# Performance work log

Hardware: AMD Instinct MI355X
Metric: run time of the kernel (lower is better)

The kernel has to match this reference:

```python
import jax, jax.numpy as jnp
import numpy as np

N_HEAD = 16
N_EMBD = 1024


def setup_inputs() -> dict:
    key = jax.random.key(0)
    k1, k2 = jax.random.split(key)
    x = jax.random.normal(k1, (2, 2048, N_EMBD), dtype=jnp.float32)
    # nn.Linear(n_embd, 3*n_embd, bias=False); store as [in, out] for x @ w
    w_qkv = jax.random.normal(k2, (N_EMBD, 3 * N_EMBD), dtype=jnp.float32) * (N_EMBD ** -0.5)
    return {"x": x, "w_qkv": w_qkv}


def reference(x, w_qkv):
    B, T, C = x.shape
    H = N_HEAD
    D = C // H  # head dim
    qkv = x @ w_qkv  # [B, T, 3C]
    q, k, v = jnp.split(qkv, 3, axis=2)
    # [B, T, H, D] -> [B, H, T, D]
    q = q.reshape(B, T, H, D).transpose(0, 2, 1, 3)
    k = k.reshape(B, T, H, D).transpose(0, 2, 1, 3)
    v = v.reshape(B, T, H, D).transpose(0, 2, 1, 3)
    att = jnp.einsum('bhtd,bhsd->bhts', q, k) / np.sqrt(D).astype(np.float32)
    causal = jnp.tril(jnp.ones((T, T), dtype=bool))  # [T, T]
    att = jnp.where(causal, att, -jnp.inf)
    att = jax.nn.softmax(att, axis=-1)
    out = jnp.einsum('bhts,bhsd->bhtd', att, v)  # [B, H, T, D]
    return out.transpose(0, 2, 1, 3).reshape(B, T, C)
```

## Files before the change

### kernel.cpp

```cpp
#include <hip/hip_runtime.h>
#include <hip/hip_bf16.h>

#define BATCH 2
#define SEQ   2048
#define EMBD  1024
#define NHEAD 16
#define HDIM  64
#define N3    3072
#define MTOT  4096
#define KDIM  1024

typedef __attribute__((ext_vector_type(8))) short  short8;
typedef __attribute__((ext_vector_type(4))) short  s16x4;
typedef __attribute__((ext_vector_type(4))) float  f32x4;

__device__ __forceinline__ short f2bfs(float f) {
    return __builtin_bit_cast(short, __float2bfloat16(f));
}

__global__ __launch_bounds__(256) void cast_x_kernel(const float* __restrict__ x,
                                                     short* __restrict__ xb, int n4) {
    int i = blockIdx.x * 256 + threadIdx.x;
    if (i >= n4) return;
    float4 f = reinterpret_cast<const float4*>(x)[i];
    s16x4 o;
    o[0] = f2bfs(f.x); o[1] = f2bfs(f.y);
    o[2] = f2bfs(f.z); o[3] = f2bfs(f.w);
    reinterpret_cast<s16x4*>(xb)[i] = o;
}

__global__ __launch_bounds__(256) void cast_wt_kernel(const float* __restrict__ w,
                                                      short* __restrict__ wt) {
    __shared__ float tile[32][33];
    int n0 = blockIdx.x * 32;
    int k0 = blockIdx.y * 32;
    int tx = threadIdx.x & 31;
    int ty = threadIdx.x >> 5;
#pragma unroll
    for (int i = 0; i < 4; ++i)
        tile[ty + i * 8][tx] = w[(size_t)(k0 + ty + i * 8) * N3 + n0 + tx];
    __syncthreads();
#pragma unroll
    for (int i = 0; i < 4; ++i)
        wt[(size_t)(n0 + ty + i * 8) * KDIM + k0 + tx] = f2bfs(tile[tx][ty + i * 8]);
}

__device__ __forceinline__ void stage_tile(const short* gbase, short* lbase, int tid) {
#pragma unroll
    for (int c = 0; c < 2; ++c) {
        int row = c * 64 + (tid >> 2);
        int chunk = (tid & 3) ^ ((row >> 1) & 3);
        const short* gp = gbase + (size_t)row * KDIM + chunk * 8;
        short* lp = lbase + c * 2048 + tid * 8;
        __builtin_amdgcn_global_load_lds((const __attribute__((address_space(1))) void*)gp,
                                         (__attribute__((address_space(3))) void*)lp,
                                         16, 0, 0);
    }
}

__global__ __launch_bounds__(256) void qkv_gemm_kernel(const short* __restrict__ xb,
                                                       const short* __restrict__ wt,
                                                       short* __restrict__ qb,
                                                       short* __restrict__ kbuf,
                                                       short* __restrict__ vt) {
    __shared__ short lA[2][128 * 32];
    __shared__ short lB[2][128 * 32];

    const int tid  = threadIdx.x;
    const int lane = tid & 63;
    const int wid  = tid >> 6;
    const int wm = wid >> 1, wn = wid & 1;
    const int lid = blockIdx.x;
    const int swz = (lid & 7) * 96 + (lid >> 3);
    const int m0 = (swz / 24) * 128;
    const int n0 = (swz % 24) * 128;

    f32x4 acc[4][4];
#pragma unroll
    for (int i = 0; i < 4; ++i)
#pragma unroll
        for (int j = 0; j < 4; ++j) acc[i][j] = (f32x4){0.f, 0.f, 0.f, 0.f};

    const short* gA = xb + (size_t)m0 * KDIM;
    const short* gB = wt + (size_t)n0 * KDIM;

    stage_tile(gA, lA[0], tid);
    stage_tile(gB, lB[0], tid);

    int cur = 0;
    const int arow = (lane & 15) * 32 + (((lane >> 4) ^ ((lane >> 1) & 3)) * 8);
#pragma unroll 1
    for (int kt = 0; kt < KDIM / 32; ++kt) {
        if (kt + 1 < KDIM / 32) {
            stage_tile(gA + (kt + 1) * 32, lA[cur ^ 1], tid);
            stage_tile(gB + (kt + 1) * 32, lB[cur ^ 1], tid);
            asm volatile("s_waitcnt vmcnt(4)" ::: "memory");
        } else {
            asm volatile("s_waitcnt vmcnt(0)" ::: "memory");
        }
        __builtin_amdgcn_s_barrier();
        __builtin_amdgcn_sched_barrier(0);
        short8 a[4], b[4];
#pragma unroll
        for (int im = 0; im < 4; ++im)
            a[im] = *(const short8*)&lA[cur][(wm * 64 + im * 16) * 32 + arow];
#pragma unroll
        for (int in = 0; in < 4; ++in)
            b[in] = *(const short8*)&lB[cur][(wn * 64 + in * 16) * 32 + arow];
#pragma unroll
        for (int im = 0; im < 4; ++im)
#pragma unroll
            for (int in = 0; in < 4; ++in)
                acc[im][in] = __builtin_amdgcn_mfma_f32_16x16x32_bf16(a[im], b[in], acc[im][in], 0, 0, 0);
        __builtin_amdgcn_sched_barrier(0);
        __builtin_amdgcn_s_barrier();
        cur ^= 1;
    }

#pragma unroll
    for (int im = 0; im < 4; ++im) {
        int t0m = m0 + wm * 64 + im * 16 + (lane >> 4) * 4;
        int b = t0m >> 11;
        int t0 = t0m & 2047;
#pragma unroll
        for (int in = 0; in < 4; ++in) {
            int col = n0 + wn * 64 + in * 16 + (lane & 15);
            int which = col >> 10;
            int h = (col >> 6) & 15;
            int d = col & 63;
            if (which == 2) {
                s16x4 pk;
#pragma unroll
                for (int r = 0; r < 4; ++r) pk[r] = f2bfs(acc[im][in][r]);
                *(s16x4*)&vt[((size_t)(b * NHEAD + h) * HDIM + d) * SEQ + t0] = pk;
            } else {
                short* dst = (which == 0) ? qb : kbuf;
                float sc = (which == 0) ? 0.125f : 1.0f;
#pragma unroll
                for (int r = 0; r < 4; ++r)
                    dst[((size_t)(b * NHEAD + h) * SEQ + t0 + r) * HDIM + d] = f2bfs(acc[im][in][r] * sc);
            }
        }
    }
}

#define KVB 128

__device__ __forceinline__ int swzf(int r) { return (r & 3) ^ (((r >> 2) & 3) << 1); }

__device__ __forceinline__ void stage_kv(const short* kh, const short* vh, int kb,
                                         short* lk, short* lv, int tid) {
#pragma unroll
    for (int c = 0; c < 2; ++c) {
        int row = c * 64 + (tid >> 3);
        int sch = (tid & 7) ^ swzf(row);
        const short* gk = kh + (size_t)(kb + row) * HDIM + sch * 8;
        __builtin_amdgcn_global_load_lds((const __attribute__((address_space(1))) void*)gk,
                                         (__attribute__((address_space(3))) void*)(lk + c * 4096 + tid * 8), 16, 0, 0);
    }
#pragma unroll
    for (int c = 0; c < 2; ++c) {
        int d = c * 32 + (tid >> 4);
        int sch = (tid & 15) ^ (d & 7);
        const short* gv = vh + (size_t)d * SEQ + kb + sch * 8;
        __builtin_amdgcn_global_load_lds((const __attribute__((address_space(1))) void*)gv,
                                         (__attribute__((address_space(3))) void*)(lv + c * 4096 + tid * 8), 16, 0, 0);
    }
}

struct AttnState {
    f32x4 o[4];
    float mrun, lrun;
};

__device__ __forceinline__ void compute_tile(const short* lk, const short* lv, int kb,
                                             int qbase, int qrow, int rbase, int hi,
                                             const short8* aQ, const short8& vone,
                                             AttnState& st) {
    const float L2E = 1.4426950408889634f;
    f32x4 s[8];
    __builtin_amdgcn_s_setprio(1);
#pragma unroll
    for (int nb = 0; nb < 8; ++nb) {
        int kidx = (nb & 3) * 32 + (rbase >> 2) * 8 + (nb >> 2) * 4 + (rbase & 3);
        f32x4 a = (f32x4){0.f, 0.f, 0.f, 0.f};
#pragma unroll
        for (int c = 0; c < 2; ++c) {
            int slot2 = (c * 4 + hi) ^ swzf(kidx);
            short8 bK = *(const short8*)&lk[kidx * 64 + slot2 * 8];
            a = __builtin_amdgcn_mfma_f32_16x16x32_bf16(bK, aQ[c], a, 0, 0, 0);
        }
        s[nb] = a;
    }
    __builtin_amdgcn_s_setprio(0);
    if (kb + KVB - 1 > qbase) {
#pragma unroll
        for (int nb = 0; nb < 8; ++nb) {
            int keyb = kb + (nb & 3) * 32 + hi * 8 + (nb >> 2) * 4;
#pragma unroll
            for (int r = 0; r < 4; ++r)
                if (keyb + r > qrow) s[nb][r] = -1e30f;
        }
    }
    float pm = -INFINITY;
#pragma unroll
    for (int nb = 0; nb < 8; ++nb)
        pm = fmaxf(pm, fmaxf(fmaxf(s[nb][0], s[nb][1]), fmaxf(s[nb][2], s[nb][3])));
    pm = fmaxf(pm, __shfl_xor(pm, 16));
    pm = fmaxf(pm, __shfl_xor(pm, 32));
    if (__any(pm > st.mrun + 8.0f)) {
        float mnew = fmaxf(st.mrun, pm);
        float sf = exp2f((st.mrun - mnew) * L2E);
        st.mrun = mnew;
        st.lrun *= sf;
#pragma unroll
        for (int dt = 0; dt < 4; ++dt)
#pragma unroll
            for (int r = 0; r < 4; ++r) st.o[dt][r] *= sf;
    }
    float mterm = st.mrun * L2E;
    short8 bp[4];
#pragma unroll
    for (int c = 0; c < 4; ++c)
#pragma unroll
        for (int jj = 0; jj < 8; ++jj) {
            float p = exp2f(fmaf(s[c + (jj >> 2) * 4][jj & 3], L2E, -mterm));
            bp[c][jj] = f2bfs(p);
        }
    f32x4 osum = (f32x4){0.f, 0.f, 0.f, 0.f};
    __builtin_amdgcn_s_setprio(1);
#pragma unroll
    for (int dt = 0; dt < 4; ++dt) {
        int d = dt * 16 + rbase;
#pragma unroll
        for (int c = 0; c < 4; ++c) {
            int slot2 = (c * 4 + hi) ^ (d & 7);
            short8 bV = *(const short8*)&lv[d * 128 + slot2 * 8];
            st.o[dt] = __builtin_amdgcn_mfma_f32_16x16x32_bf16(bV, bp[c], st.o[dt], 0, 0, 0);
        }
    }
#pragma unroll
    for (int c = 0; c < 4; ++c)
        osum = __builtin_amdgcn_mfma_f32_16x16x32_bf16(vone, bp[c], osum, 0, 0, 0);
    __builtin_amdgcn_s_setprio(0);
    st.lrun += osum[0];
}

__global__ __launch_bounds__(512, 4) void attn_kernel(const short* __restrict__ q,
                                                      const short* __restrict__ kk,
                                                      const short* __restrict__ vtg,
                                                      float* __restrict__ out) {
    const int tid  = threadIdx.x;
    const int lane = tid & 63;
    const int wid  = tid >> 6;
    const int lid  = blockIdx.x;
    const int xcd  = lid & 7;
    const int v    = lid >> 3;
    const int h4   = v & 3;
    const int ps   = (v >> 2) & 7;
    const int half = v >> 5;
    const int qt   = half ? ps : (15 - ps);
    const int bh   = h4 * 8 + xcd;
    const int rbase = lane & 15;
    const int hi    = lane >> 4;

    const short* qh = q   + (size_t)bh * SEQ * HDIM;
    const short* kh = kk  + (size_t)bh * SEQ * HDIM;
    const short* vh = vtg + (size_t)bh * HDIM * SEQ;

    __shared__ short lK[2][KVB * 64];
    __shared__ short lV[2][HDIM * KVB];

    short8 vone;
#pragma unroll
    for (int jj = 0; jj < 8; ++jj) vone[jj] = (short)0x3F80;

    const int b = bh >> 4, h = bh & 15;

    const int qbase = qt * 128 + wid * 16;
    const int qrow  = qbase + rbase;

    short8 aQ[2];
#pragma unroll
    for (int c = 0; c < 2; ++c)
        aQ[c] = *(const short8*)&qh[(size_t)qrow * HDIM + c * 32 + hi * 8];

    AttnState st;
#pragma unroll
    for (int i = 0; i < 4; ++i) st.o[i] = (f32x4){0.f, 0.f, 0.f, 0.f};
    st.mrun = -INFINITY;
    st.lrun = 0.f;

    const int ktiles = qt + 1;
    stage_kv(kh, vh, 0, lK[0], lV[0], tid);
#pragma unroll 1
    for (int t = 0; t < ktiles; t += 2) {
        {
            const int kb = t * KVB;
            if (t + 1 < ktiles) {
                stage_kv(kh, vh, kb + KVB, lK[1], lV[1], tid);
                asm volatile("s_waitcnt vmcnt(4)" ::: "memory");
            } else {
                asm volatile("s_waitcnt vmcnt(0)" ::: "memory");
            }
            __builtin_amdgcn_s_barrier();
            __builtin_amdgcn_sched_barrier(0);
            if (kb < qbase + 16)
                compute_tile(lK[0], lV[0], kb, qbase, qrow, rbase, hi, aQ, vone, st);
            __builtin_amdgcn_sched_barrier(0);
            __builtin_amdgcn_s_barrier();
        }
        if (t + 1 < ktiles) {
            const int kb = (t + 1) * KVB;
            if (t + 2 < ktiles) {
                stage_kv(kh, vh, kb + KVB, lK[0], lV[0], tid);
                asm volatile("s_waitcnt vmcnt(4)" ::: "memory");
            } else {
                asm volatile("s_waitcnt vmcnt(0)" ::: "memory");
            }
            __builtin_amdgcn_s_barrier();
            __builtin_amdgcn_sched_barrier(0);
            if (kb < qbase + 16)
                compute_tile(lK[1], lV[1], kb, qbase, qrow, rbase, hi, aQ, vone, st);
            __builtin_amdgcn_sched_barrier(0);
            __builtin_amdgcn_s_barrier();
        }
    }

    float inv = 1.0f / st.lrun;
#pragma unroll
    for (int dt = 0; dt < 4; ++dt) {
        f32x4 ov;
#pragma unroll
        for (int r = 0; r < 4; ++r) ov[r] = st.o[dt][r] * inv;
        *(f32x4*)&out[((size_t)(b * SEQ + qrow) * NHEAD + h) * HDIM + dt * 16 + hi * 4] = ov;
    }
}

extern "C" void kernel_launch(void* const* d_in, const int* in_sizes, int n_in,
                              void* d_out, int out_size, void* d_ws, size_t ws_size,
                              hipStream_t stream) {
    const float* x = (const float*)d_in[0];
    const float* w = (const float*)d_in[1];
    float* out = (float*)d_out;

    char* ws = (char*)d_ws;
    short* xb   = (short*)(ws);
    short* wt   = (short*)(ws + (size_t)8  * 1024 * 1024);
    short* qb   = (short*)(ws + (size_t)14 * 1024 * 1024);
    short* kbuf = (short*)(ws + (size_t)22 * 1024 * 1024);
    short* vt   = (short*)(ws + (size_t)30 * 1024 * 1024);

    cast_x_kernel<<<dim3(MTOT * KDIM / 4 / 256), dim3(256), 0, stream>>>(x, xb, MTOT * KDIM / 4);
    cast_wt_kernel<<<dim3(N3 / 32, KDIM / 32), dim3(256), 0, stream>>>(w, wt);
    qkv_gemm_kernel<<<dim3(768), dim3(256), 0, stream>>>(xb, wt, qb, kbuf, vt);
    attn_kernel<<<dim3(512), dim3(512), 0, stream>>>(qb, kbuf, vt, out);
}
```

Before: 90.40 us.

## Enlarge QKV GEMM tiles to 256x256x64 with 8 waves and interleaved prefetch

Rewrites the QKV projection GEMM to use 256x256 output tiles with a K-step of 64, 512 threads (8 waves, each owning 128x64), and XOR-swizzled LDS staging. Prefetch of the next K-tile is split into four chunks interleaved with MFMA groups, and s_setprio raises priority around the math. The goal is more data reuse per LDS load and fewer blocks. The trade-off is that only 192 blocks are launched, fewer than two waves' worth across the CUs, and the larger LDS footprint (128KB) limits occupancy.

```diff
diff --git a/kernel.cpp b/kernel.cpp
--- a/kernel.cpp
+++ b/kernel.cpp
@@ -45,100 +45,137 @@
         wt[(size_t)(n0 + ty + i * 8) * KDIM + k0 + tx] = f2bfs(tile[tx][ty + i * 8]);
 }
 
-__device__ __forceinline__ void stage_tile(const short* gbase, short* lbase, int tid) {
-#pragma unroll
-    for (int c = 0; c < 2; ++c) {
-        int row = c * 64 + (tid >> 2);
-        int chunk = (tid & 3) ^ ((row >> 1) & 3);
-        const short* gp = gbase + (size_t)row * KDIM + chunk * 8;
-        short* lp = lbase + c * 2048 + tid * 8;
+__device__ __forceinline__ void stage_q(const short* gsrc, short* ldst, int tid) {
+    const int lane = tid & 63, wd = tid >> 6;
+#pragma unroll
+    for (int l = 0; l < 2; ++l) {
+        int row = l * 64 + wd * 8 + (lane >> 3);
+        int chunk = (lane & 7) ^ (lane >> 3);
+        const short* gp = gsrc + (size_t)row * KDIM + chunk * 8;
+        short* lp = ldst + l * 4096 + wd * 512 + lane * 8;
         __builtin_amdgcn_global_load_lds((const __attribute__((address_space(1))) void*)gp,
-                                         (__attribute__((address_space(3))) void*)lp,
-                                         16, 0, 0);
-    }
-}
-
-__global__ __launch_bounds__(256) void qkv_gemm_kernel(const short* __restrict__ xb,
-                                                       const short* __restrict__ wt,
-                                                       short* __restrict__ qb,
-                                                       short* __restrict__ kbuf,
-                                                       short* __restrict__ vt) {
-    __shared__ short lA[2][128 * 32];
-    __shared__ short lB[2][128 * 32];
+                                         (__attribute__((address_space(3))) void*)lp, 16, 0, 0);
+    }
+}
+
+__global__ __launch_bounds__(512, 2) void qkv_gemm_kernel(const short* __restrict__ xb,
+                                                          const short* __restrict__ wt,
+                                                          short* __restrict__ qb,
+                                                          short* __restrict__ kbuf,
+                                                          short* __restrict__ vt) {
+    __shared__ short lA[2][256 * 64];
+    __shared__ short lB[2][256 * 64];
 
     const int tid  = threadIdx.x;
     const int lane = tid & 63;
     const int wid  = tid >> 6;
-    const int wm = wid >> 1, wn = wid & 1;
+    const int wm = wid >> 2, wn = wid & 3;
+    const int rbase = lane & 15;
+    const int hi    = lane >> 4;
     const int lid = blockIdx.x;
-    const int swz = (lid & 7) * 96 + (lid >> 3);
-    const int m0 = (swz / 24) * 128;
-    const int n0 = (swz % 24) * 128;
-
-    f32x4 acc[4][4];
-#pragma unroll
-    for (int i = 0; i < 4; ++i)
+    const int swz = (lid & 7) * 24 + (lid >> 3);
+    const int m0 = (swz / 12) * 256;
+    const int n0 = (swz % 12) * 256;
+
+    f32x4 acc[8][4];
+#pragma unroll
+    for (int i = 0; i < 8; ++i)
 #pragma unroll
         for (int j = 0; j < 4; ++j) acc[i][j] = (f32x4){0.f, 0.f, 0.f, 0.f};
 
     const short* gA = xb + (size_t)m0 * KDIM;
     const short* gB = wt + (size_t)n0 * KDIM;
 
-    stage_tile(gA, lA[0], tid);
-    stage_tile(gB, lB[0], tid);
-
-    int cur = 0;
-    const int arow = (lane & 15) * 32 + (((lane >> 4) ^ ((lane >> 1) & 3)) * 8);
+#pragma unroll
+    for (int q = 0; q < 4; ++q)
+        stage_q((q < 2 ? gA + (size_t)q * 128 * KDIM : gB + (size_t)(q - 2) * 128 * KDIM),
+                (q < 2 ? &lA[0][q * 8192] : &lB[0][(q - 2) * 8192]), tid);
+
+    const int aslot = ((0 * 4 + hi) ^ (rbase & 7));
+
 #pragma unroll 1
-    for (int kt = 0; kt < KDIM / 32; ++kt) {
-        if (kt + 1 < KDIM / 32) {
-            stage_tile(gA + (kt + 1) * 32, lA[cur ^ 1], tid);
-            stage_tile(gB + (kt + 1) * 32, lB[cur ^ 1], tid);
-            asm volatile("s_waitcnt vmcnt(4)" ::: "memory");
-        } else {
-            asm volatile("s_waitcnt vmcnt(0)" ::: "memory");
-        }
-        __builtin_amdgcn_s_barrier();
-        __builtin_amdgcn_sched_barrier(0);
-        short8 a[4], b[4];
-#pragma unroll
-        for (int im = 0; im < 4; ++im)
-            a[im] = *(const short8*)&lA[cur][(wm * 64 + im * 16) * 32 + arow];
-#pragma unroll
-        for (int in = 0; in < 4; ++in)
-            b[in] = *(const short8*)&lB[cur][(wn * 64 + in * 16) * 32 + arow];
-#pragma unroll
-        for (int im = 0; im < 4; ++im)
-#pragma unroll
-            for (int in = 0; in < 4; ++in)
-                acc[im][in] = __builtin_amdgcn_mfma_f32_16x16x32_bf16(a[im], b[in], acc[im][in], 0, 0, 0);
+    for (int kt = 0; kt < KDIM / 64; ++kt) {
+        const int cb = kt & 1;
+        const short* lAc = lA[cb];
+        const short* lBc = lB[cb];
+        short* lAn = lA[cb ^ 1];
+        short* lBn = lB[cb ^ 1];
+        short8 bfr[4][2];
+#pragma unroll
+        for (int p = 0; p < 4; ++p) {
+            if (kt + 1 < KDIM / 64) {
+                const short* gsrc = (p < 2) ? gA + (size_t)p * 128 * KDIM + (kt + 1) * 64
+                                            : gB + (size_t)(p - 2) * 128 * KDIM + (kt + 1) * 64;
+                short* ldst = (p < 2) ? lAn + p * 8192 : lBn + (p - 2) * 8192;
+                stage_q(gsrc, ldst, tid);
+            }
+            if (p == 0) {
+                if (kt + 1 < KDIM / 64) {
+                    asm volatile("s_waitcnt vmcnt(2)" ::: "memory");
+                } else {
+                    asm volatile("s_waitcnt vmcnt(0)" ::: "memory");
+                }
+                __builtin_amdgcn_s_barrier();
+                __builtin_amdgcn_sched_barrier(0);
+#pragma unroll
+                for (int fj = 0; fj < 4; ++fj) {
+#pragma unroll
+                    for (int kk = 0; kk < 2; ++kk) {
+                        int row = wn * 64 + fj * 16 + rbase;
+                        int slot = (kk * 4 + hi) ^ (rbase & 7);
+                        bfr[fj][kk] = *(const short8*)&lBc[row * 64 + slot * 8];
+                    }
+                }
+            }
+            short8 afr[2][2];
+#pragma unroll
+            for (int i = 0; i < 2; ++i)
+#pragma unroll
+                for (int kk = 0; kk < 2; ++kk) {
+                    int row = wm * 128 + (2 * p + i) * 16 + rbase;
+                    int slot = (kk * 4 + hi) ^ (rbase & 7);
+                    afr[i][kk] = *(const short8*)&lAc[row * 64 + slot * 8];
+                }
+            asm volatile("s_waitcnt lgkmcnt(0)" ::: "memory");
+            __builtin_amdgcn_sched_barrier(0);
+            __builtin_amdgcn_s_setprio(1);
+#pragma unroll
+            for (int i = 0; i < 2; ++i)
+#pragma unroll
+                for (int fj = 0; fj < 4; ++fj)
+#pragma unroll
+                    for (int kk = 0; kk < 2; ++kk)
+                        acc[2 * p + i][fj] = __builtin_amdgcn_mfma_f32_16x16x32_bf16(
+                            afr[i][kk], bfr[fj][kk], acc[2 * p + i][fj], 0, 0, 0);
+            __builtin_amdgcn_s_setprio(0);
+        }
         __builtin_amdgcn_sched_barrier(0);
         __builtin_amdgcn_s_barrier();
-        cur ^= 1;
-    }
-
-#pragma unroll
-    for (int im = 0; im < 4; ++im) {
-        int t0m = m0 + wm * 64 + im * 16 + (lane >> 4) * 4;
+    }
+    (void)aslot;
+
+#pragma unroll
+    for (int fi = 0; fi < 8; ++fi) {
+        int t0m = m0 + wm * 128 + fi * 16 + hi * 4;
         int b = t0m >> 11;
         int t0 = t0m & 2047;
 #pragma unroll
-        for (int in = 0; in < 4; ++in) {
-            int col = n0 + wn * 64 + in * 16 + (lane & 15);
+        for (int fj = 0; fj < 4; ++fj) {
+            int col = n0 + wn * 64 + fj * 16 + rbase;
             int which = col >> 10;
             int h = (col >> 6) & 15;
             int d = col & 63;
             if (which == 2) {
                 s16x4 pk;
 #pragma unroll
-                for (int r = 0; r < 4; ++r) pk[r] = f2bfs(acc[im][in][r]);
+                for (int r = 0; r < 4; ++r) pk[r] = f2bfs(acc[fi][fj][r]);
                 *(s16x4*)&vt[((size_t)(b * NHEAD + h) * HDIM + d) * SEQ + t0] = pk;
             } else {
                 short* dst = (which == 0) ? qb : kbuf;
                 float sc = (which == 0) ? 0.125f : 1.0f;
 #pragma unroll
                 for (int r = 0; r < 4; ++r)
-                    dst[((size_t)(b * NHEAD + h) * SEQ + t0 + r) * HDIM + d] = f2bfs(acc[im][in][r] * sc);
+                    dst[((size_t)(b * NHEAD + h) * SEQ + t0 + r) * HDIM + d] = f2bfs(acc[fi][fj][r] * sc);
             }
         }
     }
@@ -353,6 +390,6 @@
 
     cast_x_kernel<<<dim3(MTOT * KDIM / 4 / 256), dim3(256), 0, stream>>>(x, xb, MTOT * KDIM / 4);
     cast_wt_kernel<<<dim3(N3 / 32, KDIM / 32), dim3(256), 0, stream>>>(w, wt);
-    qkv_gemm_kernel<<<dim3(768), dim3(256), 0, stream>>>(xb, wt, qb, kbuf, vt);
+    qkv_gemm_kernel<<<dim3(192), dim3(512), 0, stream>>>(xb, wt, qb, kbuf, vt);
     attn_kernel<<<dim3(512), dim3(512), 0, stream>>>(qb, kbuf, vt, out);
 }
```

New measurement: 100.9 us. 11.6% more time.
